# Optimization experiments

Hardware: AMD Instinct MI355X
Metric: run time of the kernel (lower is better)

## Reference

```python
import jax, jax.numpy as jnp
import numpy as np

N = 50000
E = 800000
IN_DIM = 128
HID = 64
HEADS = 4
NUM_CLASSES = 2
NEG_SLOPE = 0.2  # PyG GATConv default


def gat_conv(x, src, dst, W, att_src, att_dst, bias, concat):
    """PyG-style GATConv (inference). src/dst include self-loops.
    x: [N, F_in]; W: [F_in, H*C]; att_*: [H, C]; bias: [H*C] or [C]."""
    n = x.shape[0]
    H, C = att_src.shape
    xl = (x @ W).reshape(n, H, C)                      # [N,H,C]
    a_s = jnp.einsum('nhc,hc->nh', xl, att_src)        # [N,H]
    a_d = jnp.einsum('nhc,hc->nh', xl, att_dst)
    alpha = jax.nn.leaky_relu(a_s[src] + a_d[dst], NEG_SLOPE)  # [E,H]
    # segment softmax over destination nodes (stable)
    m = jax.ops.segment_max(alpha, dst, num_segments=n)
    m = jnp.where(jnp.isfinite(m), m, 0.0)
    e = jnp.exp(alpha - m[dst])
    s = jax.ops.segment_sum(e, dst, num_segments=n)
    a = e / (s[dst] + 1e-16)                           # [E,H]
    out = jax.ops.segment_sum(a[:, :, None] * xl[src], dst, num_segments=n)  # [N,H,C]
    out = out.reshape(n, H * C) if concat else out.mean(axis=1)
    return out + bias


def setup_inputs() -> dict:
    key = jax.random.key(0)
    ks = jax.random.split(key, 16)
    g = lambda k, shp, fan: jax.random.normal(k, shp, jnp.float32) * (1.0 / np.sqrt(fan))
    x = jax.random.normal(ks[0], (N, IN_DIM), jnp.float32)
    edge_index = jax.random.randint(ks[1], (2, E), 0, N, jnp.int64)
    return {
        'x': x, 'edge_index': edge_index,
        'W1': g(ks[2], (IN_DIM, HEADS * HID), IN_DIM),
        'att_src1': g(ks[3], (HEADS, HID), HID), 'att_dst1': g(ks[4], (HEADS, HID), HID),
        'b1': jnp.zeros((HEADS * HID,), jnp.float32),
        'W2': g(ks[5], (HEADS * HID, HEADS * HID), HEADS * HID),
        'att_src2': g(ks[6], (HEADS, HID), HID), 'att_dst2': g(ks[7], (HEADS, HID), HID),
        'b2': jnp.zeros((HEADS * HID,), jnp.float32),
        'W3': g(ks[8], (HEADS * HID, HID), HEADS * HID),
        'att_src3': g(ks[9], (1, HID), HID), 'att_dst3': g(ks[10], (1, HID), HID),
        'b3': jnp.zeros((HID,), jnp.float32),
        'fc_w': g(ks[11], (HID, NUM_CLASSES), HID),
        'fc_b': jnp.zeros((NUM_CLASSES,), jnp.float32),
    }


def reference(x, edge_index, W1, att_src1, att_dst1, b1, W2, att_src2, att_dst2, b2,
              W3, att_src3, att_dst3, b3, fc_w, fc_b):
    n = x.shape[0]
    loops = jnp.arange(n, dtype=edge_index.dtype)
    src = jnp.concatenate([edge_index[0], loops])  # add_self_loops=True (PyG default)
    dst = jnp.concatenate([edge_index[1], loops])
    h = gat_conv(x, src, dst, W1, att_src1, att_dst1, b1, concat=True)
    h = jax.nn.elu(h)
    h = gat_conv(h, src, dst, W2, att_src2, att_dst2, b2, concat=True)
    h = jax.nn.elu(h)
    h = gat_conv(h, src, dst, W3, att_src3, att_dst3, b3, concat=False)
    return h @ fc_w + fc_b
```

## Files before the change

### kernel.cpp

```cpp
#include <hip/hip_runtime.h>
#include <hip/hip_fp16.h>
#include <math.h>

#define N_NODES 50000
#define N_EDGES 800000
#define ETOT (N_EDGES + N_NODES)
#define IN_DIM 128
#define HIDC 64
#define HEADS 4
#define F1 (HEADS * HIDC)
#define MP 50048
#define SCAN_BLOCKS 196

#define WOFF1 0
#define WOFF2 32768
#define WOFF3 98304
#define WTOT_ITEMS 14336

typedef _Float16 f16x8 __attribute__((ext_vector_type(8)));
typedef float f32x4 __attribute__((ext_vector_type(4)));
typedef unsigned short u16x8 __attribute__((ext_vector_type(8)));

__device__ inline unsigned short f2h_bits(float f) {
  _Float16 h = (_Float16)f;
  return __builtin_bit_cast(unsigned short, h);
}
__device__ inline float h_bits2f(unsigned short b) {
  return (float)__builtin_bit_cast(_Float16, b);
}

__device__ inline void gload_lds16(const void* g, void* l) {
  __builtin_amdgcn_global_load_lds(
      (const __attribute__((address_space(1))) unsigned int*)g,
      (__attribute__((address_space(3))) unsigned int*)l, 16, 0, 0);
}

__global__ void detect_init_kernel(const unsigned int* __restrict__ buf, int* __restrict__ flag,
                                   int* __restrict__ cnt, int* __restrict__ fillc) {
  int i = blockIdx.x * blockDim.x + threadIdx.x;
  if (i < N_NODES) { cnt[i] = 1; fillc[i] = 0; }
  if (blockIdx.x == 0) {
    __shared__ int any;
    if (threadIdx.x == 0) any = 0;
    __syncthreads();
    for (int k = threadIdx.x; k < 2048; k += blockDim.x)
      if (buf[2 * k + 1] != 0u) any = 1;
    __syncthreads();
    if (threadIdx.x == 0) *flag = any;
  }
}

__global__ void decode_hist_kernel(const void* __restrict__ eidx, const int* __restrict__ flag,
                                   int* __restrict__ srcO, int* __restrict__ dstO,
                                   int* __restrict__ cnt) {
  int i = blockIdx.x * blockDim.x + threadIdx.x;
  if (i >= N_EDGES) return;
  int s, d;
  if (*flag) {
    const int* b = (const int*)eidx;
    s = b[i]; d = b[N_EDGES + i];
  } else {
    const long long* b = (const long long*)eidx;
    s = (int)b[i]; d = (int)b[N_EDGES + i];
  }
  srcO[i] = s;
  dstO[i] = d;
  atomicAdd(&cnt[d], 1);
}

__global__ __launch_bounds__(256) void scan1_kernel(const int* __restrict__ cnt,
                                                    int* __restrict__ escan,
                                                    int* __restrict__ bsum) {
  __shared__ int tmp[256];
  const int t = threadIdx.x;
  const int i = blockIdx.x * 256 + t;
  int v = (i < N_NODES) ? cnt[i] : 0;
  tmp[t] = v;
  __syncthreads();
#pragma unroll
  for (int o = 1; o < 256; o <<= 1) {
    int u = (t >= o) ? tmp[t - o] : 0;
    __syncthreads();
    tmp[t] += u;
    __syncthreads();
  }
  if (i < N_NODES) escan[i] = tmp[t] - v;
  if (t == 255) bsum[blockIdx.x] = tmp[255];
}

__global__ __launch_bounds__(256) void scan2_kernel(const int* __restrict__ bsum,
                                                    int* __restrict__ boff) {
  __shared__ int tmp[256];
  const int t = threadIdx.x;
  int v = (t < SCAN_BLOCKS) ? bsum[t] : 0;
  tmp[t] = v;
  __syncthreads();
#pragma unroll
  for (int o = 1; o < 256; o <<= 1) {
    int u = (t >= o) ? tmp[t - o] : 0;
    __syncthreads();
    tmp[t] += u;
    __syncthreads();
  }
  if (t < SCAN_BLOCKS) boff[t] = tmp[t] - v;
}

__global__ __launch_bounds__(256) void scan3_kernel(const int* __restrict__ escan,
                                                    const int* __restrict__ boff,
                                                    int* __restrict__ off) {
  const int i = blockIdx.x * 256 + threadIdx.x;
  if (i < N_NODES) off[i] = escan[i] + boff[blockIdx.x];
  if (i == 0) off[N_NODES] = ETOT;
}

__global__ void fill_kernel(const int* __restrict__ src, const int* __restrict__ dst,
                            const int* __restrict__ csrOff, int* __restrict__ fillc,
                            int* __restrict__ csrSrc) {
  int i = blockIdx.x * blockDim.x + threadIdx.x;
  if (i >= ETOT) return;
  int s, d;
  if (i < N_EDGES) { s = src[i]; d = dst[i]; } else { s = i - N_EDGES; d = s; }
  int pos = csrOff[d] + atomicAdd(&fillc[d], 1);
  csrSrc[pos] = s;
}

template <int K>
__global__ __launch_bounds__(256) void convA_kernel(const float* __restrict__ A,
                                                    unsigned short* __restrict__ At, int M) {
  __shared__ float ld[16][264];
  const int mblk = blockIdx.x;
  const int tid = threadIdx.x;
  const int elems = 16 * K;
#pragma unroll
  for (int e = tid * 4; e < elems; e += 1024) {
    int r = e / K, c = e % K;
    int row = mblk * 16 + r;
    float4 v = make_float4(0.f, 0.f, 0.f, 0.f);
    if (row < M) v = *reinterpret_cast<const float4*>(&A[(size_t)row * K + c]);
    ld[r][c + 0] = v.x; ld[r][c + 1] = v.y; ld[r][c + 2] = v.z; ld[r][c + 3] = v.w;
  }
  __syncthreads();
#pragma unroll
  for (int o = tid * 8; o < elems; o += 2048) {
    int r = (o >> 3) & 15;
    int kg = (o >> 7) & 3;
    int kb = o >> 9;
    int k0 = kb * 32 + kg * 8;
    u16x8 h8;
#pragma unroll
    for (int j = 0; j < 8; ++j) h8[j] = f2h_bits(ld[r][k0 + j]);
    size_t base = ((size_t)mblk * (K >> 5) + kb) * 512 + (size_t)(kg * 16 + r) * 8;
    *reinterpret_cast<u16x8*>(At + base) = h8;
  }
}

__device__ inline void convW_item(const float* __restrict__ W, int K, int Nw, int t,
                                  unsigned short* __restrict__ hi, unsigned short* __restrict__ lo) {
  int KB = K >> 5;
  int c = t & 15;
  int kg = (t >> 4) & 3;
  int kb = (t >> 6) % KB;
  int nblk = (t >> 6) / KB;
  int n = nblk * 16 + c;
  int k0 = kb * 32 + kg * 8;
  u16x8 h8, l8;
#pragma unroll
  for (int j = 0; j < 8; ++j) {
    float v = W[(size_t)(k0 + j) * Nw + n];
    unsigned short h = f2h_bits(v);
    h8[j] = h;
    l8[j] = f2h_bits(v - h_bits2f(h));
  }
  *reinterpret_cast<u16x8*>(hi + (size_t)t * 8) = h8;
  *reinterpret_cast<u16x8*>(lo + (size_t)t * 8) = l8;
}

__global__ void convW_all_kernel(const float* __restrict__ W1, const float* __restrict__ W2,
                                 const float* __restrict__ W3,
                                 unsigned short* __restrict__ hi, unsigned short* __restrict__ lo) {
  int t = blockIdx.x * blockDim.x + threadIdx.x;
  if (t >= WTOT_ITEMS) return;
  if (t < 4096) {
    convW_item(W1, IN_DIM, F1, t, hi + WOFF1, lo + WOFF1);
  } else if (t < 4096 + 8192) {
    convW_item(W2, F1, F1, t - 4096, hi + WOFF2, lo + WOFF2);
  } else {
    convW_item(W3, F1, HIDC, t - (4096 + 8192), hi + WOFF3, lo + WOFF3);
  }
}

template <int KB, int NB, int H>
__global__ __launch_bounds__(256) void gemm_f16_kernel(
    const unsigned short* __restrict__ At,
    const unsigned short* __restrict__ Bhi, const unsigned short* __restrict__ Blo,
    const float* __restrict__ atts, const float* __restrict__ attd,
    __half* __restrict__ Ch, float* __restrict__ a_s, float* __restrict__ a_d,
    int M, int Nout) {
  __shared__ unsigned short As[8 * 512];
  __shared__ unsigned short BsH[NB * 512], BsL[NB * 512];
  const int tid = threadIdx.x;
  const int w = tid >> 6, lane = tid & 63;
  const size_t machunk = ((size_t)blockIdx.x * 8 + w * 2) * KB;
  const int nblk0 = blockIdx.y * NB;
  const int laneo = lane * 8;

  f32x4 acc[2][NB];
#pragma unroll
  for (int mi = 0; mi < 2; ++mi)
#pragma unroll
    for (int nj = 0; nj < NB; ++nj) acc[mi][nj] = {0.f, 0.f, 0.f, 0.f};

  for (int kb = 0; kb < KB; ++kb) {
    gload_lds16(At + (machunk + kb) * 512 + laneo, As + (w * 2) * 512);
    gload_lds16(At + (machunk + (size_t)KB + kb) * 512 + laneo, As + (w * 2 + 1) * 512);
#pragma unroll
    for (int q = 0; q < NB / 4; ++q) {
      int nbl = w * (NB / 4) + q;
      size_t bo = ((size_t)(nblk0 + nbl) * KB + kb) * 512 + laneo;
      gload_lds16(Bhi + bo, BsH + nbl * 512);
      gload_lds16(Blo + bo, BsL + nbl * 512);
    }
    __syncthreads();
    f16x8 a0 = *reinterpret_cast<const f16x8*>(As + (w * 2) * 512 + laneo);
    f16x8 a1 = *reinterpret_cast<const f16x8*>(As + (w * 2 + 1) * 512 + laneo);
#pragma unroll
    for (int nj = 0; nj < NB; ++nj) {
      f16x8 bh = *reinterpret_cast<const f16x8*>(BsH + nj * 512 + laneo);
      f16x8 bl = *reinterpret_cast<const f16x8*>(BsL + nj * 512 + laneo);
      acc[0][nj] = __builtin_amdgcn_mfma_f32_16x16x32_f16(a0, bh, acc[0][nj], 0, 0, 0);
      acc[1][nj] = __builtin_amdgcn_mfma_f32_16x16x32_f16(a1, bh, acc[1][nj], 0, 0, 0);
      acc[0][nj] = __builtin_amdgcn_mfma_f32_16x16x32_f16(a0, bl, acc[0][nj], 0, 0, 0);
      acc[1][nj] = __builtin_amdgcn_mfma_f32_16x16x32_f16(a1, bl, acc[1][nj], 0, 0, 0);
    }
    __syncthreads();
  }
  const int col0 = nblk0 * 16 + (lane & 15);
  const int row0 = blockIdx.x * 128 + w * 32 + (lane >> 4) * 4;
  float attsv[NB], attdv[NB];
#pragma unroll
  for (int nj = 0; nj < NB; ++nj) {
    int gcol = nblk0 + nj;
    int hh = gcol >> 2;
    int coff = (gcol & 3) * 16 + (lane & 15);
    attsv[nj] = atts[hh * 64 + coff];
    attdv[nj] = attd[hh * 64 + coff];
  }
#pragma unroll
  for (int mi = 0; mi < 2; ++mi) {
#pragma unroll
    for (int nj = 0; nj < NB; ++nj) {
      int col = col0 + nj * 16;
#pragma unroll
      for (int r = 0; r < 4; ++r) {
        int row = row0 + mi * 16 + r;
        if (row < M) Ch[(size_t)row * Nout + col] = __float2half(acc[mi][nj][r]);
      }
    }
#pragma unroll
    for (int r = 0; r < 4; ++r) {
      int row = row0 + mi * 16 + r;
#pragma unroll
      for (int g = 0; g < NB / 4; ++g) {
        float ps = 0.f, pd = 0.f;
#pragma unroll
        for (int q = 0; q < 4; ++q) {
          float v = acc[mi][g * 4 + q][r];
          ps = fmaf(v, attsv[g * 4 + q], ps);
          pd = fmaf(v, attdv[g * 4 + q], pd);
        }
#pragma unroll
        for (int o = 1; o <= 8; o <<= 1) {
          ps += __shfl_xor(ps, o);
          pd += __shfl_xor(pd, o);
        }
        if ((lane & 15) == 0 && row < M) {
          int hh = (nblk0 + g * 4) >> 2;
          a_s[(size_t)row * H + hh] = ps;
          a_d[(size_t)row * H + hh] = pd;
        }
      }
    }
  }
}

__global__ __launch_bounds__(256) void gat_agg4_kernel(const __half* __restrict__ xlh,
                                                       const float* __restrict__ a_srcv,
                                                       const float* __restrict__ a_dstv,
                                                       const int* __restrict__ csrOff,
                                                       const int* __restrict__ csrSrc,
                                                       const float* __restrict__ bias,
                                                       unsigned short* __restrict__ outT) {
  __shared__ float4 plds[4][64];
  __shared__ int slds[4][64];
  const int w = threadIdx.x >> 6;
  const int lane = threadIdx.x & 63;
  const int d = blockIdx.x * 4 + w;
  if (d >= N_NODES) return;
  const int h = lane >> 4;
  int e0 = csrOff[d], e1 = csrOff[d + 1];
  float4 adv = reinterpret_cast<const float4*>(a_dstv)[d];
  float m[4], ssum[4];
#pragma unroll
  for (int j = 0; j < 4; ++j) { m[j] = -1e30f; ssum[j] = 0.f; }
  float4 acc = make_float4(0.f, 0.f, 0.f, 0.f);
  const float* pbase = reinterpret_cast<const float*>(&plds[w][0]);

  for (int cb = e0; cb < e1; cb += 64) {
    int ecount = min(64, e1 - cb);
    int sidx = (lane < ecount) ? csrSrc[cb + lane] : 0;
    slds[w][lane] = sidx;
    float4 asv = make_float4(0.f, 0.f, 0.f, 0.f);
    if (lane < ecount) asv = reinterpret_cast<const float4*>(a_srcv)[sidx];
    float p[4], scl[4];
#pragma unroll
    for (int j = 0; j < 4; ++j) {
      float av = (j == 0) ? asv.x : (j == 1) ? asv.y : (j == 2) ? asv.z : asv.w;
      float dv = (j == 0) ? adv.x : (j == 1) ? adv.y : (j == 2) ? adv.z : adv.w;
      float al = -1e30f;
      if (lane < ecount) {
        float v = av + dv;
        al = (v > 0.f) ? v : 0.2f * v;
      }
      float cm = al;
#pragma unroll
      for (int o = 32; o > 0; o >>= 1) cm = fmaxf(cm, __shfl_xor(cm, o));
      float nm = fmaxf(m[j], cm);
      float scale = __expf(m[j] - nm);
      p[j] = (lane < ecount) ? __expf(al - nm) : 0.f;
      float ps = p[j];
#pragma unroll
      for (int o = 32; o > 0; o >>= 1) ps += __shfl_xor(ps, o);
      ssum[j] = ssum[j] * scale + ps;
      m[j] = nm;
      scl[j] = scale;
    }
    plds[w][lane] = make_float4(p[0], p[1], p[2], p[3]);
    float sc = (h == 0) ? scl[0] : (h == 1) ? scl[1] : (h == 2) ? scl[2] : scl[3];
    acc.x *= sc; acc.y *= sc; acc.z *= sc; acc.w *= sc;
    for (int i = 0; i < ecount; ++i) {
      int s = slds[w][i];
      float pv = pbase[i * 4 + h];
      uint2 raw = *reinterpret_cast<const uint2*>(xlh + (size_t)s * 256 + lane * 4);
      float2 f0 = __half22float2(__builtin_bit_cast(__half2, raw.x));
      float2 f1 = __half22float2(__builtin_bit_cast(__half2, raw.y));
      acc.x = fmaf(pv, f0.x, acc.x);
      acc.y = fmaf(pv, f0.y, acc.y);
      acc.z = fmaf(pv, f1.x, acc.z);
      acc.w = fmaf(pv, f1.y, acc.w);
    }
  }
  float sm = (h == 0) ? ssum[0] : (h == 1) ? ssum[1] : (h == 2) ? ssum[2] : ssum[3];
  float inv = 1.f / (sm + 1e-16f);
  float4 bv = reinterpret_cast<const float4*>(bias)[lane];
  float4 r;
  r.x = acc.x * inv + bv.x;
  r.y = acc.y * inv + bv.y;
  r.z = acc.z * inv + bv.z;
  r.w = acc.w * inv + bv.w;
  r.x = (r.x > 0.f) ? r.x : (__expf(r.x) - 1.f);
  r.y = (r.y > 0.f) ? r.y : (__expf(r.y) - 1.f);
  r.z = (r.z > 0.f) ? r.z : (__expf(r.z) - 1.f);
  r.w = (r.w > 0.f) ? r.w : (__expf(r.w) - 1.f);
  ushort4 hh;
  hh.x = f2h_bits(r.x);
  hh.y = f2h_bits(r.y);
  hh.z = f2h_bits(r.z);
  hh.w = f2h_bits(r.w);
  const int mblk = d >> 4, rr = d & 15;
  const int kb = lane >> 3, kg = (lane >> 1) & 3, jj = (lane & 1) * 4;
  size_t base = ((size_t)mblk * 8 + kb) * 512 + (size_t)(kg * 16 + rr) * 8 + jj;
  *reinterpret_cast<ushort4*>(outT + base) = hh;
}

__global__ __launch_bounds__(256) void gat_final_kernel(const __half* __restrict__ xlh,
                                                        const float* __restrict__ a_srcv,
                                                        const float* __restrict__ a_dstv,
                                                        const int* __restrict__ csrOff,
                                                        const int* __restrict__ csrSrc,
                                                        const float* __restrict__ b3,
                                                        const float* __restrict__ fcw,
                                                        const float* __restrict__ fcb,
                                                        float* __restrict__ out) {
  __shared__ float plds[4][64];
  __shared__ int slds[4][64];
  const int w = threadIdx.x >> 6;
  const int lane = threadIdx.x & 63;
  const int d = blockIdx.x * 4 + w;
  if (d >= N_NODES) return;
  const int g = lane >> 4;
  const int c4 = lane & 15;
  int e0 = csrOff[d], e1 = csrOff[d + 1];
  float adv = a_dstv[d];
  float m = -1e30f, ssum = 0.f;
  float4 acc = make_float4(0.f, 0.f, 0.f, 0.f);

  for (int cb = e0; cb < e1; cb += 64) {
    int ecount = min(64, e1 - cb);
    int sidx = (lane < ecount) ? csrSrc[cb + lane] : 0;
    slds[w][lane] = sidx;
    float al = -1e30f;
    if (lane < ecount) {
      float v = a_srcv[sidx] + adv;
      al = (v > 0.f) ? v : 0.2f * v;
    }
    float cm = al;
#pragma unroll
    for (int o = 32; o > 0; o >>= 1) cm = fmaxf(cm, __shfl_xor(cm, o));
    float nm = fmaxf(m, cm);
    float scale = __expf(m - nm);
    float p = (lane < ecount) ? __expf(al - nm) : 0.f;
    float ps = p;
#pragma unroll
    for (int o = 32; o > 0; o >>= 1) ps += __shfl_xor(ps, o);
    ssum = ssum * scale + ps;
    m = nm;
    plds[w][lane] = p;
    acc.x *= scale; acc.y *= scale; acc.z *= scale; acc.w *= scale;
    for (int i = 0; i < ecount; i += 4) {
      int e = i + g;
      int s = slds[w][e];
      float pv = plds[w][e];
      uint2 raw = *reinterpret_cast<const uint2*>(xlh + (size_t)s * 64 + c4 * 4);
      float2 f0 = __half22float2(__builtin_bit_cast(__half2, raw.x));
      float2 f1 = __half22float2(__builtin_bit_cast(__half2, raw.y));
      acc.x = fmaf(pv, f0.x, acc.x);
      acc.y = fmaf(pv, f0.y, acc.y);
      acc.z = fmaf(pv, f1.x, acc.z);
      acc.w = fmaf(pv, f1.y, acc.w);
    }
  }
#pragma unroll
  for (int o = 16; o <= 32; o <<= 1) {
    acc.x += __shfl_xor(acc.x, o);
    acc.y += __shfl_xor(acc.y, o);
    acc.z += __shfl_xor(acc.z, o);
    acc.w += __shfl_xor(acc.w, o);
  }
  float inv = 1.f / (ssum + 1e-16f);
  float4 bv = reinterpret_cast<const float4*>(b3)[c4];
  float4 v;
  v.x = acc.x * inv + bv.x;
  v.y = acc.y * inv + bv.y;
  v.z = acc.z * inv + bv.z;
  v.w = acc.w * inv + bv.w;
  const float2* fcw2 = reinterpret_cast<const float2*>(fcw);
  float2 w0 = fcw2[c4 * 4 + 0], w1 = fcw2[c4 * 4 + 1], w2 = fcw2[c4 * 4 + 2], w3 = fcw2[c4 * 4 + 3];
  float l0 = v.x * w0.x + v.y * w1.x + v.z * w2.x + v.w * w3.x;
  float l1 = v.x * w0.y + v.y * w1.y + v.z * w2.y + v.w * w3.y;
#pragma unroll
  for (int o = 1; o <= 8; o <<= 1) {
    l0 += __shfl_xor(l0, o);
    l1 += __shfl_xor(l1, o);
  }
  if (lane == 0) {
    out[2 * d + 0] = l0 + fcb[0];
    out[2 * d + 1] = l1 + fcb[1];
  }
}

extern "C" void kernel_launch(void* const* d_in, const int* in_sizes, int n_in,
                              void* d_out, int out_size, void* d_ws, size_t ws_size,
                              hipStream_t stream) {
  (void)in_sizes; (void)n_in; (void)out_size; (void)ws_size;
  const float* x      = (const float*)d_in[0];
  const void*  eidx   = d_in[1];
  const float* W1     = (const float*)d_in[2];
  const float* att_s1 = (const float*)d_in[3];
  const float* att_d1 = (const float*)d_in[4];
  const float* b1     = (const float*)d_in[5];
  const float* W2     = (const float*)d_in[6];
  const float* att_s2 = (const float*)d_in[7];
  const float* att_d2 = (const float*)d_in[8];
  const float* b2     = (const float*)d_in[9];
  const float* W3     = (const float*)d_in[10];
  const float* att_s3 = (const float*)d_in[11];
  const float* att_d3 = (const float*)d_in[12];
  const float* b3     = (const float*)d_in[13];
  const float* fcw    = (const float*)d_in[14];
  const float* fcb    = (const float*)d_in[15];
  float* out = (float*)d_out;

  char* ws = (char*)d_ws;
  size_t off = 0;
  auto alloc = [&](size_t bytes) -> void* {
    void* p = (void*)(ws + off);
    off += (bytes + 255) & ~(size_t)255;
    return p;
  };
  int*   srcI   = (int*)alloc((size_t)N_EDGES * 4);
  int*   dstI   = (int*)alloc((size_t)N_EDGES * 4);
  int*   cnt    = (int*)alloc((size_t)N_NODES * 4);
  int*   fillc  = (int*)alloc((size_t)N_NODES * 4);
  int*   csrOff = (int*)alloc((size_t)(N_NODES + 1) * 4);
  int*   csrSrc = (int*)alloc((size_t)ETOT * 4);
  int*   flag   = (int*)alloc(256);
  int*   escan  = (int*)alloc((size_t)N_NODES * 4);
  int*   bsum   = (int*)alloc((size_t)SCAN_BLOCKS * 4);
  int*   boff   = (int*)alloc((size_t)SCAN_BLOCKS * 4);
  float* a_s    = (float*)alloc((size_t)N_NODES * HEADS * 4);
  float* a_d    = (float*)alloc((size_t)N_NODES * HEADS * 4);
  unsigned short* At  = (unsigned short*)alloc((size_t)MP * F1 * 2);
  unsigned short* Whi = (unsigned short*)alloc((size_t)(WOFF3 + 16384) * 2);
  unsigned short* Wlo = (unsigned short*)alloc((size_t)(WOFF3 + 16384) * 2);
  __half* xlh  = (__half*)alloc((size_t)MP * F1 * 2);
  __half* xlh3 = (__half*)alloc((size_t)MP * HIDC * 2);

  detect_init_kernel<<<(N_NODES + 255) / 256, 256, 0, stream>>>((const unsigned int*)eidx, flag, cnt, fillc);
  decode_hist_kernel<<<(N_EDGES + 255) / 256, 256, 0, stream>>>(eidx, flag, srcI, dstI, cnt);
  scan1_kernel<<<SCAN_BLOCKS, 256, 0, stream>>>(cnt, escan, bsum);
  scan2_kernel<<<1, 256, 0, stream>>>(bsum, boff);
  scan3_kernel<<<SCAN_BLOCKS, 256, 0, stream>>>(escan, boff, csrOff);
  fill_kernel<<<(ETOT + 255) / 256, 256, 0, stream>>>(srcI, dstI, csrOff, fillc, csrSrc);
  convW_all_kernel<<<(WTOT_ITEMS + 255) / 256, 256, 0, stream>>>(W1, W2, W3, Whi, Wlo);

  const int gn = (N_NODES + 3) / 4;
  const int gmb = MP / 16;
  const int gx = MP / 128;

  convA_kernel<IN_DIM><<<gmb, 256, 0, stream>>>(x, At, N_NODES);
  gemm_f16_kernel<4, 8, 4><<<dim3(gx, 2), 256, 0, stream>>>(At, Whi + WOFF1, Wlo + WOFF1,
                                                            att_s1, att_d1, xlh, a_s, a_d, N_NODES, F1);
  gat_agg4_kernel<<<gn, 256, 0, stream>>>(xlh, a_s, a_d, csrOff, csrSrc, b1, At);

  gemm_f16_kernel<8, 8, 4><<<dim3(gx, 2), 256, 0, stream>>>(At, Whi + WOFF2, Wlo + WOFF2,
                                                            att_s2, att_d2, xlh, a_s, a_d, N_NODES, F1);
  gat_agg4_kernel<<<gn, 256, 0, stream>>>(xlh, a_s, a_d, csrOff, csrSrc, b2, At);

  gemm_f16_kernel<8, 4, 1><<<dim3(gx, 1), 256, 0, stream>>>(At, Whi + WOFF3, Wlo + WOFF3,
                                                            att_s3, att_d3, xlh3, a_s, a_d, N_NODES, HIDC);
  gat_final_kernel<<<gn, 256, 0, stream>>>(xlh3, a_s, a_d, csrOff, csrSrc, b3, fcw, fcb, out);
}
```

Before: 354.7 us.

## Fuse setup kernels and remap GAT aggregation softmax to edge-by-head lanes

The edge-index detect/init kernel and the weight hi/lo conversion kernel become one launch, selected by block range. The scan2 and scan3 kernels are merged: every block redundantly scans the block sums and then applies its own offset. The layer-1/2 aggregation kernel now processes 16-edge chunks with lanes mapped as edge by head, so each lane handles one head for the online softmax. This replaces the four per-lane heads reduced over 64 lanes, aiming to cut shuffle work and idle lanes at an average degree near 17. Per-head scales and sums are passed between lanes through LDS, which adds small shared-memory traffic and some redundant scan work per block.

```diff
diff --git a/kernel.cpp b/kernel.cpp
--- a/kernel.cpp
+++ b/kernel.cpp
@@ -16,6 +16,7 @@
 #define WOFF2 32768
 #define WOFF3 98304
 #define WTOT_ITEMS 14336
+#define CONVW_BLOCKS 56
 
 typedef _Float16 f16x8 __attribute__((ext_vector_type(8)));
 typedef float f32x4 __attribute__((ext_vector_type(4)));
@@ -35,18 +36,54 @@
       (__attribute__((address_space(3))) unsigned int*)l, 16, 0, 0);
 }
 
-__global__ void detect_init_kernel(const unsigned int* __restrict__ buf, int* __restrict__ flag,
-                                   int* __restrict__ cnt, int* __restrict__ fillc) {
-  int i = blockIdx.x * blockDim.x + threadIdx.x;
-  if (i < N_NODES) { cnt[i] = 1; fillc[i] = 0; }
-  if (blockIdx.x == 0) {
-    __shared__ int any;
-    if (threadIdx.x == 0) any = 0;
-    __syncthreads();
-    for (int k = threadIdx.x; k < 2048; k += blockDim.x)
-      if (buf[2 * k + 1] != 0u) any = 1;
-    __syncthreads();
-    if (threadIdx.x == 0) *flag = any;
+__device__ inline void convW_item(const float* __restrict__ W, int K, int Nw, int t,
+                                  unsigned short* __restrict__ hi, unsigned short* __restrict__ lo) {
+  int KB = K >> 5;
+  int c = t & 15;
+  int kg = (t >> 4) & 3;
+  int kb = (t >> 6) % KB;
+  int nblk = (t >> 6) / KB;
+  int n = nblk * 16 + c;
+  int k0 = kb * 32 + kg * 8;
+  u16x8 h8, l8;
+#pragma unroll
+  for (int j = 0; j < 8; ++j) {
+    float v = W[(size_t)(k0 + j) * Nw + n];
+    unsigned short h = f2h_bits(v);
+    h8[j] = h;
+    l8[j] = f2h_bits(v - h_bits2f(h));
+  }
+  *reinterpret_cast<u16x8*>(hi + (size_t)t * 8) = h8;
+  *reinterpret_cast<u16x8*>(lo + (size_t)t * 8) = l8;
+}
+
+__global__ void detect_init_convw_kernel(const unsigned int* __restrict__ buf, int* __restrict__ flag,
+                                         int* __restrict__ cnt, int* __restrict__ fillc,
+                                         const float* __restrict__ W1, const float* __restrict__ W2,
+                                         const float* __restrict__ W3,
+                                         unsigned short* __restrict__ hi, unsigned short* __restrict__ lo) {
+  if (blockIdx.x < SCAN_BLOCKS) {
+    int i = blockIdx.x * 256 + threadIdx.x;
+    if (i < N_NODES) { cnt[i] = 1; fillc[i] = 0; }
+    if (blockIdx.x == 0) {
+      __shared__ int any;
+      if (threadIdx.x == 0) any = 0;
+      __syncthreads();
+      for (int k = threadIdx.x; k < 2048; k += blockDim.x)
+        if (buf[2 * k + 1] != 0u) any = 1;
+      __syncthreads();
+      if (threadIdx.x == 0) *flag = any;
+    }
+  } else {
+    int t = (blockIdx.x - SCAN_BLOCKS) * 256 + threadIdx.x;
+    if (t >= WTOT_ITEMS) return;
+    if (t < 4096) {
+      convW_item(W1, IN_DIM, F1, t, hi + WOFF1, lo + WOFF1);
+    } else if (t < 4096 + 8192) {
+      convW_item(W2, F1, F1, t - 4096, hi + WOFF2, lo + WOFF2);
+    } else {
+      convW_item(W3, F1, HIDC, t - (4096 + 8192), hi + WOFF3, lo + WOFF3);
+    }
   }
 }
 
@@ -88,8 +125,9 @@
   if (t == 255) bsum[blockIdx.x] = tmp[255];
 }
 
-__global__ __launch_bounds__(256) void scan2_kernel(const int* __restrict__ bsum,
-                                                    int* __restrict__ boff) {
+__global__ __launch_bounds__(256) void scan23_kernel(const int* __restrict__ escan,
+                                                     const int* __restrict__ bsum,
+                                                     int* __restrict__ off) {
   __shared__ int tmp[256];
   const int t = threadIdx.x;
   int v = (t < SCAN_BLOCKS) ? bsum[t] : 0;
@@ -102,14 +140,9 @@
     tmp[t] += u;
     __syncthreads();
   }
-  if (t < SCAN_BLOCKS) boff[t] = tmp[t] - v;
-}
-
-__global__ __launch_bounds__(256) void scan3_kernel(const int* __restrict__ escan,
-                                                    const int* __restrict__ boff,
-                                                    int* __restrict__ off) {
-  const int i = blockIdx.x * 256 + threadIdx.x;
-  if (i < N_NODES) off[i] = escan[i] + boff[blockIdx.x];
+  int boff = (blockIdx.x == 0) ? 0 : tmp[blockIdx.x - 1];
+  const int i = blockIdx.x * 256 + t;
+  if (i < N_NODES) off[i] = escan[i] + boff;
   if (i == 0) off[N_NODES] = ETOT;
 }
 
@@ -151,41 +184,6 @@
     for (int j = 0; j < 8; ++j) h8[j] = f2h_bits(ld[r][k0 + j]);
     size_t base = ((size_t)mblk * (K >> 5) + kb) * 512 + (size_t)(kg * 16 + r) * 8;
     *reinterpret_cast<u16x8*>(At + base) = h8;
-  }
-}
-
-__device__ inline void convW_item(const float* __restrict__ W, int K, int Nw, int t,
-                                  unsigned short* __restrict__ hi, unsigned short* __restrict__ lo) {
-  int KB = K >> 5;
-  int c = t & 15;
-  int kg = (t >> 4) & 3;
-  int kb = (t >> 6) % KB;
-  int nblk = (t >> 6) / KB;
-  int n = nblk * 16 + c;
-  int k0 = kb * 32 + kg * 8;
-  u16x8 h8, l8;
-#pragma unroll
-  for (int j = 0; j < 8; ++j) {
-    float v = W[(size_t)(k0 + j) * Nw + n];
-    unsigned short h = f2h_bits(v);
-    h8[j] = h;
-    l8[j] = f2h_bits(v - h_bits2f(h));
-  }
-  *reinterpret_cast<u16x8*>(hi + (size_t)t * 8) = h8;
-  *reinterpret_cast<u16x8*>(lo + (size_t)t * 8) = l8;
-}
-
-__global__ void convW_all_kernel(const float* __restrict__ W1, const float* __restrict__ W2,
-                                 const float* __restrict__ W3,
-                                 unsigned short* __restrict__ hi, unsigned short* __restrict__ lo) {
-  int t = blockIdx.x * blockDim.x + threadIdx.x;
-  if (t >= WTOT_ITEMS) return;
-  if (t < 4096) {
-    convW_item(W1, IN_DIM, F1, t, hi + WOFF1, lo + WOFF1);
-  } else if (t < 4096 + 8192) {
-    convW_item(W2, F1, F1, t - 4096, hi + WOFF2, lo + WOFF2);
-  } else {
-    convW_item(W3, F1, HIDC, t - (4096 + 8192), hi + WOFF3, lo + WOFF3);
   }
 }
 
@@ -290,56 +288,50 @@
                                                        const int* __restrict__ csrSrc,
                                                        const float* __restrict__ bias,
                                                        unsigned short* __restrict__ outT) {
-  __shared__ float4 plds[4][64];
-  __shared__ int slds[4][64];
+  __shared__ float plds[4][64];
+  __shared__ int slds[4][16];
+  __shared__ float hlds[4][4];
   const int w = threadIdx.x >> 6;
   const int lane = threadIdx.x & 63;
   const int d = blockIdx.x * 4 + w;
   if (d >= N_NODES) return;
-  const int h = lane >> 4;
+  const int hG = lane >> 4;
+  const int hS = lane & 3;
+  const int eS = lane >> 2;
   int e0 = csrOff[d], e1 = csrOff[d + 1];
-  float4 adv = reinterpret_cast<const float4*>(a_dstv)[d];
-  float m[4], ssum[4];
-#pragma unroll
-  for (int j = 0; j < 4; ++j) { m[j] = -1e30f; ssum[j] = 0.f; }
+  float4 advv = reinterpret_cast<const float4*>(a_dstv)[d];
+  float adv = (hS == 0) ? advv.x : (hS == 1) ? advv.y : (hS == 2) ? advv.z : advv.w;
+  float m = -1e30f, ssum = 0.f;
   float4 acc = make_float4(0.f, 0.f, 0.f, 0.f);
-  const float* pbase = reinterpret_cast<const float*>(&plds[w][0]);
-
-  for (int cb = e0; cb < e1; cb += 64) {
-    int ecount = min(64, e1 - cb);
-    int sidx = (lane < ecount) ? csrSrc[cb + lane] : 0;
-    slds[w][lane] = sidx;
-    float4 asv = make_float4(0.f, 0.f, 0.f, 0.f);
-    if (lane < ecount) asv = reinterpret_cast<const float4*>(a_srcv)[sidx];
-    float p[4], scl[4];
-#pragma unroll
-    for (int j = 0; j < 4; ++j) {
-      float av = (j == 0) ? asv.x : (j == 1) ? asv.y : (j == 2) ? asv.z : asv.w;
-      float dv = (j == 0) ? adv.x : (j == 1) ? adv.y : (j == 2) ? adv.z : adv.w;
-      float al = -1e30f;
-      if (lane < ecount) {
-        float v = av + dv;
-        al = (v > 0.f) ? v : 0.2f * v;
-      }
-      float cm = al;
-#pragma unroll
-      for (int o = 32; o > 0; o >>= 1) cm = fmaxf(cm, __shfl_xor(cm, o));
-      float nm = fmaxf(m[j], cm);
-      float scale = __expf(m[j] - nm);
-      p[j] = (lane < ecount) ? __expf(al - nm) : 0.f;
-      float ps = p[j];
-#pragma unroll
-      for (int o = 32; o > 0; o >>= 1) ps += __shfl_xor(ps, o);
-      ssum[j] = ssum[j] * scale + ps;
-      m[j] = nm;
-      scl[j] = scale;
-    }
-    plds[w][lane] = make_float4(p[0], p[1], p[2], p[3]);
-    float sc = (h == 0) ? scl[0] : (h == 1) ? scl[1] : (h == 2) ? scl[2] : scl[3];
+  const float* pbase = &plds[w][0];
+
+  for (int cb = e0; cb < e1; cb += 16) {
+    int ecount = min(16, e1 - cb);
+    int sidx = (eS < ecount) ? csrSrc[cb + eS] : 0;
+    float al = -1e30f;
+    if (eS < ecount) {
+      float v = a_srcv[sidx * 4 + hS] + adv;
+      al = (v > 0.f) ? v : 0.2f * v;
+    }
+    float cm = al;
+#pragma unroll
+    for (int o = 4; o <= 32; o <<= 1) cm = fmaxf(cm, __shfl_xor(cm, o));
+    float nm = fmaxf(m, cm);
+    float scale = __expf(m - nm);
+    float p = (eS < ecount) ? __expf(al - nm) : 0.f;
+    float ps = p;
+#pragma unroll
+    for (int o = 4; o <= 32; o <<= 1) ps += __shfl_xor(ps, o);
+    ssum = ssum * scale + ps;
+    m = nm;
+    plds[w][eS * 4 + hS] = p;
+    if (eS == 0) hlds[w][hS] = scale;
+    if (hS == 0) slds[w][eS] = sidx;
+    float sc = hlds[w][hG];
     acc.x *= sc; acc.y *= sc; acc.z *= sc; acc.w *= sc;
     for (int i = 0; i < ecount; ++i) {
       int s = slds[w][i];
-      float pv = pbase[i * 4 + h];
+      float pv = pbase[i * 4 + hG];
       uint2 raw = *reinterpret_cast<const uint2*>(xlh + (size_t)s * 256 + lane * 4);
       float2 f0 = __half22float2(__builtin_bit_cast(__half2, raw.x));
       float2 f1 = __half22float2(__builtin_bit_cast(__half2, raw.y));
@@ -349,7 +341,8 @@
       acc.w = fmaf(pv, f1.y, acc.w);
     }
   }
-  float sm = (h == 0) ? ssum[0] : (h == 1) ? ssum[1] : (h == 2) ? ssum[2] : ssum[3];
+  if (eS == 0) hlds[w][hS] = ssum;
+  float sm = hlds[w][hG];
   float inv = 1.f / (sm + 1e-16f);
   float4 bv = reinterpret_cast<const float4*>(bias)[lane];
   float4 r;
@@ -496,7 +489,6 @@
   int*   flag   = (int*)alloc(256);
   int*   escan  = (int*)alloc((size_t)N_NODES * 4);
   int*   bsum   = (int*)alloc((size_t)SCAN_BLOCKS * 4);
-  int*   boff   = (int*)alloc((size_t)SCAN_BLOCKS * 4);
   float* a_s    = (float*)alloc((size_t)N_NODES * HEADS * 4);
   float* a_d    = (float*)alloc((size_t)N_NODES * HEADS * 4);
   unsigned short* At  = (unsigned short*)alloc((size_t)MP * F1 * 2);
@@ -505,13 +497,12 @@
   __half* xlh  = (__half*)alloc((size_t)MP * F1 * 2);
   __half* xlh3 = (__half*)alloc((size_t)MP * HIDC * 2);
 
-  detect_init_kernel<<<(N_NODES + 255) / 256, 256, 0, stream>>>((const unsigned int*)eidx, flag, cnt, fillc);
+  detect_init_convw_kernel<<<SCAN_BLOCKS + CONVW_BLOCKS, 256, 0, stream>>>(
+      (const unsigned int*)eidx, flag, cnt, fillc, W1, W2, W3, Whi, Wlo);
   decode_hist_kernel<<<(N_EDGES + 255) / 256, 256, 0, stream>>>(eidx, flag, srcI, dstI, cnt);
   scan1_kernel<<<SCAN_BLOCKS, 256, 0, stream>>>(cnt, escan, bsum);
-  scan2_kernel<<<1, 256, 0, stream>>>(bsum, boff);
-  scan3_kernel<<<SCAN_BLOCKS, 256, 0, stream>>>(escan, boff, csrOff);
+  scan23_kernel<<<SCAN_BLOCKS, 256, 0, stream>>>(escan, bsum, csrOff);
   fill_kernel<<<(ETOT + 255) / 256, 256, 0, stream>>>(srcI, dstI, csrOff, fillc, csrSrc);
-  convW_all_kernel<<<(WTOT_ITEMS + 255) / 256, 256, 0, stream>>>(W1, W2, W3, Whi, Wlo);
 
   const int gn = (N_NODES + 3) / 4;
   const int gmb = MP / 16;
```

Result: faster. 340.8 us (-3.9%).
